# Performance work log

Measured on AMD Instinct MI355X. Metric: run time of the kernel, lower is better.

The kernel has to match this reference:

```python
import jax, jax.numpy as jnp
import numpy as np

B, MODES, L = 512, 1000, 64


def setup_inputs() -> dict:
    key = jax.random.key(0)
    ks = jax.random.split(key, 10)
    inp = {
        "params": jax.random.normal(ks[0], (B, MODES, L), dtype=jnp.float32),
        "wfft0_re": jax.random.uniform(ks[1], (L, MODES), dtype=jnp.float32),
        "wfft0_im": jax.random.uniform(ks[2], (L, MODES), dtype=jnp.float32),
        "wfft1_re": jax.random.uniform(ks[3], (L, MODES), dtype=jnp.float32),
        "wfft1_im": jax.random.uniform(ks[4], (L, MODES), dtype=jnp.float32),
        "wfft2_re": jax.random.uniform(ks[5], (L, MODES), dtype=jnp.float32),
        "wfft2_im": jax.random.uniform(ks[6], (L, MODES), dtype=jnp.float32),
        "lin1_w": jax.random.normal(ks[7], (MODES, L * MODES), dtype=jnp.float32) * 0.01,
        "lin1_b": jnp.zeros((MODES,), dtype=jnp.float32),
        "lin2_w": jax.random.normal(ks[8], (L, MODES), dtype=jnp.float32) * 0.05,
        "lin2_b": jnp.zeros((L,), dtype=jnp.float32),
    }
    return inp


def _stft_block(x, wfft):
    # x: (B, MODES, L) real or complex; wfft: (L, MODES) complex
    fx = jnp.fft.fft(x, norm="forward")            # FFT over last (layer) axis, scaled 1/L
    # Faithful to torch.einsum('bfp,mn->bfm', ...): sums over BOTH p and n
    y = jnp.einsum("bfp,mn->bfm", fx, wfft)         # (B, MODES, L)
    y = jnp.fft.ifft(y, norm="forward")             # unnormalized inverse (norm='forward')
    return jnp.tanh(y).real                         # complex tanh, then real part


def reference(params, wfft0_re, wfft0_im, wfft1_re, wfft1_im, wfft2_re, wfft2_im,
              lin1_w, lin1_b, lin2_w, lin2_b):
    w0 = wfft0_re + 1j * wfft0_im
    w1 = wfft1_re + 1j * wfft1_im
    w2 = wfft2_re + 1j * wfft2_im
    x = _stft_block(params, w0)
    x = _stft_block(x, w1)
    x = _stft_block(x, w2)
    x = x.reshape(x.shape[0], -1)                   # (B, MODES*L), row-major like torch.flatten
    x = jnp.tanh(x @ lin1_w.T + lin1_b)             # (B, MODES)
    x = jax.nn.sigmoid(x @ lin2_w.T + lin2_b)       # (B, L)
    return x
```

## Files before the change

kernel.cpp:

```cpp
#include <hip/hip_runtime.h>
#include <math.h>

#define NB 512
#define MODES 1000
#define LL 64
#define PI_D 3.14159265358979323846

#define OFF_PART   0
#define OFF_SCAL   4096
#define OFF_T2RE   4224
#define OFF_T2IM   4736
#define OFF_GP     5248
#define OFF_CNT    5504
#define OFF_W2T    16384
#define OFF_S2     2621440
#define OFF_IRR    4718592
#define OFF_E      6815744
#define OFF_SG     13107200
#define OFF_HP4    19398656
#define HP4_STRIDE 524288

__device__ __forceinline__ double retanh_d(double a, double b) {
    if (fabs(a) > 20.0) return a > 0.0 ? 1.0 : -1.0;
    double e2 = exp(2.0 * a);
    double em2 = 1.0 / e2;
    return (e2 - em2) / (e2 + em2 + 2.0 * cos(2.0 * b));
}

__global__ void k_misc(const float* __restrict__ w0r, const float* __restrict__ w0i,
                       const float* __restrict__ w1r, const float* __restrict__ w1i,
                       const float* __restrict__ w2r, const float* __restrict__ w2i,
                       const float* __restrict__ w2, char* ws) {
    int bid = blockIdx.x, t = threadIdx.x;
    if (bid < 192) {
        int k = bid >> 6, m = bid & 63;
        const float* wr = (k == 0) ? w0r : (k == 1) ? w1r : w2r;
        const float* wi = (k == 0) ? w0i : (k == 1) ? w1i : w2i;
        double sr = 0.0, si = 0.0;
        for (int c = t; c < MODES; c += 256) {
            sr += (double)wr[m * MODES + c];
            si += (double)wi[m * MODES + c];
        }
        __shared__ double lr[256], li[256];
        lr[t] = sr; li[t] = si; __syncthreads();
        for (int s = 128; s > 0; s >>= 1) {
            if (t < s) { lr[t] += lr[t + s]; li[t] += li[t + s]; }
            __syncthreads();
        }
        if (t == 0) {
            double2* p = (double2*)(ws + OFF_PART);
            p[k * 64 + m] = make_double2(lr[0], li[0]);
        }
    } else {
        int idx = (bid - 192) * 256 + t;
        int o = idx >> 6, j = idx & 63;
        ((float*)(ws + OFF_W2T))[idx] = w2[j * MODES + o];
    }
}

__global__ void k_prep(char* ws) {
    int t = threadIdx.x;
    int j = t & 63, q = t >> 6;
    double2* part = (double2*)(ws + OFF_PART);
    double* scal  = (double*)(ws + OFF_SCAL);
    double* t2re  = (double*)(ws + OFF_T2RE);
    double* t2im  = (double*)(ws + OFF_T2IM);
    float*  gp    = (float*)(ws + OFF_GP);
    __shared__ double a1[128], a2[128];
    __shared__ double sre[64], sim[64];
    __shared__ double tc[64], tsn[64];
    __shared__ double pr[4][64], pi_[4][64];
    if (t < 128) {
        double2 v = part[t];
        a1[t] = v.x; a2[t] = v.y;
    }
    if (t < 64) {
        double2 v = part[128 + t];
        sre[t] = v.x; sim[t] = v.y;
    }
    if (t >= 128 && t < 192) {
        int r = t - 128;
        double s, c;
        sincos((double)r * (PI_D / 32.0), &s, &c);
        tc[r] = c; tsn[r] = s;
    }
    __syncthreads();
    for (int s = 32; s > 0; s >>= 1) {
        if (t < 128 && (t & 63) < s) { a1[t] += a1[t + s]; a2[t] += a2[t + s]; }
        __syncthreads();
    }
    if (t < 2) { scal[2 * t] = a1[t * 64]; scal[2 * t + 1] = a2[t * 64]; }
    double tr = 0.0, ti = 0.0;
    for (int mm = q * 16; mm < q * 16 + 16; ++mm) {
        int r = (j * mm) & 63;
        double c = tc[r], s = tsn[r];
        tr += sre[mm] * c - sim[mm] * s;
        ti += sre[mm] * s + sim[mm] * c;
    }
    pr[q][j] = tr; pi_[q][j] = ti;
    __syncthreads();
    if (t < 64) {
        double trr = pr[0][t] + pr[1][t] + pr[2][t] + pr[3][t];
        double tii = pi_[0][t] + pi_[1][t] + pi_[2][t] + pi_[3][t];
        t2re[t] = trr; t2im[t] = tii;
        gp[t] = (float)retanh_d(trr, tii);
    }
    if (t == 0) *(int*)(ws + OFF_CNT) = 0;
}

__global__ void k_sE(const float* __restrict__ w1, const float* __restrict__ params,
                     char* ws) {
    int bid = blockIdx.x, t = threadIdx.x;
    if (bid < 1000) {
        int idx = bid * 512 + t;
        const double* scal = (const double*)(ws + OFF_SCAL);
        double c0r = scal[0], c0i = scal[1], c1r = scal[2], c1i = scal[3];
        float p0 = params[(size_t)idx * 64];
        double s1 = retanh_d((double)p0 * c0r, (double)p0 * c0i);
        float s1f = (float)s1;
        double s2 = retanh_d((double)s1f * c1r, (double)s1f * c1i);
        float s2f = (float)s2;
        float sg; bool irr = false;
        if (s2f == 1.0f)       sg = 1.0f;
        else if (s2f == -1.0f) sg = -1.0f;
        else { sg = (s2f >= 0.0f) ? 1.0f : -1.0f; irr = true; }
        ((float*)(ws + OFF_SG))[idx] = sg;
        ((float*)(ws + OFF_S2))[idx] = s2f;
        if (irr) {
            int pos = atomicAdd((int*)(ws + OFF_CNT), 1);
            ((int*)(ws + OFF_IRR))[pos] = idx;
        }
    } else {
        int e = bid - 1000;
        int o = e >> 3, x = e & 7;
        const float4* w4 = (const float4*)w1;
        const float4* gp4 = (const float4*)(ws + OFF_GP);
        float4 g = gp4[t & 15];
        float* E = (float*)(ws + OFF_E);
        size_t rowbase = (size_t)o * 16000;
        int cbase = x * 2048 + t;
#pragma unroll
        for (int k = 0; k < 4; ++k) {
            int gidx = cbase + k * 512;
            float a = 0.0f;
            if (gidx < 16000) {
                float4 v = w4[rowbase + gidx];
                a = v.x * g.x + v.y * g.y + v.z * g.z + v.w * g.w;
            }
            a += __shfl_xor(a, 1);
            a += __shfl_xor(a, 2);
            a += __shfl_xor(a, 4);
            a += __shfl_xor(a, 8);
            if ((t & 15) == 0) {
                int f = x * 128 + k * 32 + (t >> 4);
                E[(size_t)o * 1024 + f] = a;
            }
        }
    }
}

__global__ void k_gemm(char* ws) {
    __shared__ float As[32][68];
    __shared__ float Bs[32][68];
    const float* sgn = (const float*)(ws + OFF_SG);
    const float* E   = (const float*)(ws + OFF_E);
    float* hp4       = (float*)(ws + OFF_HP4);
    int bx = blockIdx.x;
    int by = blockIdx.y;
    int bz = blockIdx.z;
    int t = threadIdx.x;
    int tx = t & 15, ty = t >> 4;
    float acc[4][4] = {};
    const float4 z4 = make_float4(0.f, 0.f, 0.f, 0.f);
    for (int kt = 0; kt < 8; ++kt) {
        int f0 = bz * 256 + kt * 32;
#pragma unroll
        for (int p = 0; p < 2; ++p) {
            int r = (t >> 3) + p * 32;
            int c4 = t & 7;
            int f = f0 + c4 * 4;
            float4 v = (f < MODES) ? *(const float4*)(sgn + (size_t)(by * 64 + r) * MODES + f) : z4;
            As[c4 * 4 + 0][r] = v.x;
            As[c4 * 4 + 1][r] = v.y;
            As[c4 * 4 + 2][r] = v.z;
            As[c4 * 4 + 3][r] = v.w;
        }
#pragma unroll
        for (int p = 0; p < 2; ++p) {
            int r = (t >> 3) + p * 32;
            int c4 = t & 7;
            int o = bx * 64 + r;
            float4 v = (o < MODES) ? *(const float4*)(E + (size_t)o * 1024 + f0 + c4 * 4) : z4;
            Bs[c4 * 4 + 0][r] = v.x;
            Bs[c4 * 4 + 1][r] = v.y;
            Bs[c4 * 4 + 2][r] = v.z;
            Bs[c4 * 4 + 3][r] = v.w;
        }
        __syncthreads();
#pragma unroll
        for (int kk = 0; kk < 32; ++kk) {
            float4 a4 = *(const float4*)&As[kk][ty * 4];
            float4 b4 = *(const float4*)&Bs[kk][tx * 4];
            float av[4] = {a4.x, a4.y, a4.z, a4.w};
            float bv[4] = {b4.x, b4.y, b4.z, b4.w};
#pragma unroll
            for (int i = 0; i < 4; ++i)
#pragma unroll
                for (int j = 0; j < 4; ++j) acc[i][j] += av[i] * bv[j];
        }
        __syncthreads();
    }
    size_t zoff = (size_t)bz * HP4_STRIDE;
#pragma unroll
    for (int i = 0; i < 4; ++i) {
        int b = by * 64 + ty * 4 + i;
        float4 st = make_float4(acc[i][0], acc[i][1], acc[i][2], acc[i][3]);
        *(float4*)&hp4[zoff + (size_t)b * 1024 + bx * 64 + tx * 4] = st;
    }
}

__global__ void k_final(const float* __restrict__ w1, const float* __restrict__ b1,
                        const float* __restrict__ b2, float* __restrict__ out, char* ws) {
    int b = blockIdx.x, t = threadIdx.x;
    const float* hp4 = (const float*)(ws + OFF_HP4);
    __shared__ float h[MODES];
    __shared__ float part[4][64];
    __shared__ __align__(16) float cv[64];
    for (int o = t; o < MODES; o += 256) {
        size_t base = (size_t)b * 1024 + o;
        h[o] = hp4[base] + hp4[base + HP4_STRIDE] + hp4[base + 2 * HP4_STRIDE]
             + hp4[base + 3 * HP4_STRIDE] + b1[o];
    }
    __syncthreads();
    int cnt = *(const int*)(ws + OFF_CNT);
    if (cnt > 0) {
        const int* irr     = (const int*)(ws + OFF_IRR);
        const float* s2a   = (const float*)(ws + OFF_S2);
        const float* sgn   = (const float*)(ws + OFF_SG);
        const double* t2re = (const double*)(ws + OFF_T2RE);
        const double* t2im = (const double*)(ws + OFF_T2IM);
        const float* gp    = (const float*)(ws + OFF_GP);
        for (int e = 0; e < cnt; ++e) {
            int idx = irr[e];
            int bb = idx / 1000;
            if (bb != b) continue;
            int f = idx - bb * 1000;
            float s2 = s2a[idx];
            float sg = sgn[idx];
            if (t < 64) {
                double g = retanh_d((double)s2 * t2re[t], (double)s2 * t2im[t]);
                cv[t] = (float)g - sg * gp[t];
            }
            __syncthreads();
            const float4* w4 = (const float4*)w1;
            const float4* c4 = (const float4*)cv;
            for (int o = t; o < MODES; o += 256) {
                size_t base = (size_t)o * 16000 + (size_t)f * 16;
                float a = 0.0f;
#pragma unroll
                for (int r = 0; r < 16; ++r) {
                    float4 w = w4[base + r];
                    float4 c = c4[r];
                    a += w.x * c.x + w.y * c.y + w.z * c.z + w.w * c.w;
                }
                h[o] += a;
            }
            __syncthreads();
        }
    }
    for (int o = t; o < MODES; o += 256) h[o] = tanhf(h[o]);
    __syncthreads();
    const float* w2t = (const float*)(ws + OFF_W2T);
    int j = t & 63, c = t >> 6;
    float acc = 0.0f;
    for (int o = c * 250; o < c * 250 + 250; ++o) acc += h[o] * w2t[o * 64 + j];
    part[c][j] = acc;
    __syncthreads();
    if (t < 64) {
        float s = part[0][t] + part[1][t] + part[2][t] + part[3][t] + b2[t];
        out[b * 64 + t] = 1.0f / (1.0f + expf(-s));
    }
}

extern "C" void kernel_launch(void* const* d_in, const int* in_sizes, int n_in,
                              void* d_out, int out_size, void* d_ws, size_t ws_size,
                              hipStream_t stream) {
    const float* params = (const float*)d_in[0];
    const float* w0r = (const float*)d_in[1];
    const float* w0i = (const float*)d_in[2];
    const float* w1r = (const float*)d_in[3];
    const float* w1i = (const float*)d_in[4];
    const float* w2r = (const float*)d_in[5];
    const float* w2i = (const float*)d_in[6];
    const float* lin1w = (const float*)d_in[7];
    const float* lin1b = (const float*)d_in[8];
    const float* lin2w = (const float*)d_in[9];
    const float* lin2b = (const float*)d_in[10];
    char* ws = (char*)d_ws;
    float* out = (float*)d_out;

    k_misc<<<442, 256, 0, stream>>>(w0r, w0i, w1r, w1i, w2r, w2i, lin2w, ws);
    k_prep<<<1, 256, 0, stream>>>(ws);
    k_sE<<<9000, 512, 0, stream>>>(lin1w, params, ws);
    k_gemm<<<dim3(16, 8, 4), 256, 0, stream>>>(ws);
    k_final<<<512, 256, 0, stream>>>(lin1w, lin1b, lin2b, out, ws);
}
```

Baseline: 113.6 us.

## Replace FP32 SIMT GEMM with split-bf16 MFMA GEMM and drop split-K partials

E is stored as a hi/lo bf16 pair and the ±1 sign matrix as bf16. The GEMM now uses MFMA 16x16x32 bf16 instructions reading straight from global memory with no LDS staging, in place of the shared-memory FP32 4x4 register-tiled kernel. The 4-way split-K and the partial-sum buffer are removed, so k_final reads a single h buffer. Extra k_misc blocks zero the padding regions. This trades some precision (bf16 hi+lo ≈ 16-bit mantissa) for matrix-core throughput, on a GEMM that is small (512x1000x1000).

```diff
diff --git a/kernel.cpp b/kernel.cpp
--- a/kernel.cpp
+++ b/kernel.cpp
@@ -15,16 +15,26 @@
 #define OFF_W2T    16384
 #define OFF_S2     2621440
 #define OFF_IRR    4718592
-#define OFF_E      6815744
 #define OFF_SG     13107200
-#define OFF_HP4    19398656
-#define HP4_STRIDE 524288
+#define OFF_EHI    19398656
+#define OFF_ELO    21495808
+#define OFF_SGNB   23592960
+#define OFF_H      24641536
+
+typedef short short8 __attribute__((ext_vector_type(8)));
+typedef float f32x4 __attribute__((ext_vector_type(4)));
 
 __device__ __forceinline__ double retanh_d(double a, double b) {
     if (fabs(a) > 20.0) return a > 0.0 ? 1.0 : -1.0;
     double e2 = exp(2.0 * a);
     double em2 = 1.0 / e2;
     return (e2 - em2) / (e2 + em2 + 2.0 * cos(2.0 * b));
+}
+
+__device__ __forceinline__ unsigned short f2bf(float x) {
+    unsigned u = __float_as_uint(x);
+    unsigned r = (u + 0x7FFFu + ((u >> 16) & 1u)) >> 16;
+    return (unsigned short)r;
 }
 
 __global__ void k_misc(const float* __restrict__ w0r, const float* __restrict__ w0i,
@@ -51,10 +61,22 @@
             double2* p = (double2*)(ws + OFF_PART);
             p[k * 64 + m] = make_double2(lr[0], li[0]);
         }
-    } else {
+    } else if (bid < 442) {
         int idx = (bid - 192) * 256 + t;
         int o = idx >> 6, j = idx & 63;
         ((float*)(ws + OFF_W2T))[idx] = w2[j * MODES + o];
+    } else if (bid < 490) {
+        int idx = (bid - 442) * 256 + t;
+        ((unsigned*)(ws + OFF_EHI))[512000 + idx] = 0u;
+    } else if (bid < 538) {
+        int idx = (bid - 490) * 256 + t;
+        ((unsigned*)(ws + OFF_ELO))[512000 + idx] = 0u;
+    } else {
+        int idx = (bid - 538) * 256 + t;
+        if (idx < 6144) {
+            int b = idx / 12, u = idx % 12;
+            ((unsigned*)(ws + OFF_SGNB))[b * 512 + 500 + u] = 0u;
+        }
     }
 }
 
@@ -126,6 +148,9 @@
         else { sg = (s2f >= 0.0f) ? 1.0f : -1.0f; irr = true; }
         ((float*)(ws + OFF_SG))[idx] = sg;
         ((float*)(ws + OFF_S2))[idx] = s2f;
+        int b = idx / 1000, f = idx - b * 1000;
+        ((unsigned short*)(ws + OFF_SGNB))[(size_t)b * 1024 + f] =
+            (sg > 0.0f) ? (unsigned short)0x3F80 : (unsigned short)0xBF80;
         if (irr) {
             int pos = atomicAdd((int*)(ws + OFF_CNT), 1);
             ((int*)(ws + OFF_IRR))[pos] = idx;
@@ -136,7 +161,8 @@
         const float4* w4 = (const float4*)w1;
         const float4* gp4 = (const float4*)(ws + OFF_GP);
         float4 g = gp4[t & 15];
-        float* E = (float*)(ws + OFF_E);
+        unsigned short* ehi = (unsigned short*)(ws + OFF_EHI);
+        unsigned short* elo = (unsigned short*)(ws + OFF_ELO);
         size_t rowbase = (size_t)o * 16000;
         int cbase = x * 2048 + t;
 #pragma unroll
@@ -153,84 +179,60 @@
             a += __shfl_xor(a, 8);
             if ((t & 15) == 0) {
                 int f = x * 128 + k * 32 + (t >> 4);
-                E[(size_t)o * 1024 + f] = a;
+                unsigned short hi = f2bf(a);
+                float hif = __uint_as_float((unsigned)hi << 16);
+                unsigned short lo = f2bf(a - hif);
+                ehi[(size_t)o * 1024 + f] = hi;
+                elo[(size_t)o * 1024 + f] = lo;
             }
         }
     }
 }
 
-__global__ void k_gemm(char* ws) {
-    __shared__ float As[32][68];
-    __shared__ float Bs[32][68];
-    const float* sgn = (const float*)(ws + OFF_SG);
-    const float* E   = (const float*)(ws + OFF_E);
-    float* hp4       = (float*)(ws + OFF_HP4);
-    int bx = blockIdx.x;
-    int by = blockIdx.y;
-    int bz = blockIdx.z;
+__global__ void __launch_bounds__(128) k_gemm(char* ws) {
+    const unsigned short* sgnb = (const unsigned short*)(ws + OFF_SGNB);
+    const unsigned short* ehi  = (const unsigned short*)(ws + OFF_EHI);
+    const unsigned short* elo  = (const unsigned short*)(ws + OFF_ELO);
+    float* h = (float*)(ws + OFF_H);
+    int strip = blockIdx.x;
+    int btile = blockIdx.y;
     int t = threadIdx.x;
-    int tx = t & 15, ty = t >> 4;
-    float acc[4][4] = {};
-    const float4 z4 = make_float4(0.f, 0.f, 0.f, 0.f);
-    for (int kt = 0; kt < 8; ++kt) {
-        int f0 = bz * 256 + kt * 32;
+    int wave = t >> 6, l = t & 63;
+    int rc = l & 15, grp = l >> 4;
+    int b0 = btile * 16;
+    int o0 = strip * 64 + wave * 32;
+    f32x4 acc0 = {0.f, 0.f, 0.f, 0.f}, acc1 = {0.f, 0.f, 0.f, 0.f};
+    const unsigned short* ap  = sgnb + (size_t)(b0 + rc) * 1024 + grp * 8;
+    const unsigned short* bh0 = ehi + (size_t)(o0 + rc) * 1024 + grp * 8;
+    const unsigned short* bl0 = elo + (size_t)(o0 + rc) * 1024 + grp * 8;
+#pragma unroll 4
+    for (int s = 0; s < 32; ++s) {
+        short8 af  = *(const short8*)(ap + s * 32);
+        short8 h0  = *(const short8*)(bh0 + s * 32);
+        short8 l0  = *(const short8*)(bl0 + s * 32);
+        short8 h1  = *(const short8*)(bh0 + 16 * 1024 + s * 32);
+        short8 l1  = *(const short8*)(bl0 + 16 * 1024 + s * 32);
+        acc0 = __builtin_amdgcn_mfma_f32_16x16x32_bf16(af, h0, acc0, 0, 0, 0);
+        acc0 = __builtin_amdgcn_mfma_f32_16x16x32_bf16(af, l0, acc0, 0, 0, 0);
+        acc1 = __builtin_amdgcn_mfma_f32_16x16x32_bf16(af, h1, acc1, 0, 0, 0);
+        acc1 = __builtin_amdgcn_mfma_f32_16x16x32_bf16(af, l1, acc1, 0, 0, 0);
+    }
 #pragma unroll
-        for (int p = 0; p < 2; ++p) {
-            int r = (t >> 3) + p * 32;
-            int c4 = t & 7;
-            int f = f0 + c4 * 4;
-            float4 v = (f < MODES) ? *(const float4*)(sgn + (size_t)(by * 64 + r) * MODES + f) : z4;
-            As[c4 * 4 + 0][r] = v.x;
-            As[c4 * 4 + 1][r] = v.y;
-            As[c4 * 4 + 2][r] = v.z;
-            As[c4 * 4 + 3][r] = v.w;
-        }
-#pragma unroll
-        for (int p = 0; p < 2; ++p) {
-            int r = (t >> 3) + p * 32;
-            int c4 = t & 7;
-            int o = bx * 64 + r;
-            float4 v = (o < MODES) ? *(const float4*)(E + (size_t)o * 1024 + f0 + c4 * 4) : z4;
-            Bs[c4 * 4 + 0][r] = v.x;
-            Bs[c4 * 4 + 1][r] = v.y;
-            Bs[c4 * 4 + 2][r] = v.z;
-            Bs[c4 * 4 + 3][r] = v.w;
-        }
-        __syncthreads();
-#pragma unroll
-        for (int kk = 0; kk < 32; ++kk) {
-            float4 a4 = *(const float4*)&As[kk][ty * 4];
-            float4 b4 = *(const float4*)&Bs[kk][tx * 4];
-            float av[4] = {a4.x, a4.y, a4.z, a4.w};
-            float bv[4] = {b4.x, b4.y, b4.z, b4.w};
-#pragma unroll
-            for (int i = 0; i < 4; ++i)
-#pragma unroll
-                for (int j = 0; j < 4; ++j) acc[i][j] += av[i] * bv[j];
-        }
-        __syncthreads();
-    }
-    size_t zoff = (size_t)bz * HP4_STRIDE;
-#pragma unroll
-    for (int i = 0; i < 4; ++i) {
-        int b = by * 64 + ty * 4 + i;
-        float4 st = make_float4(acc[i][0], acc[i][1], acc[i][2], acc[i][3]);
-        *(float4*)&hp4[zoff + (size_t)b * 1024 + bx * 64 + tx * 4] = st;
+    for (int r = 0; r < 4; ++r) {
+        h[(size_t)(b0 + grp * 4 + r) * 1024 + o0 + rc]      = acc0[r];
+        h[(size_t)(b0 + grp * 4 + r) * 1024 + o0 + 16 + rc] = acc1[r];
     }
 }
 
 __global__ void k_final(const float* __restrict__ w1, const float* __restrict__ b1,
                         const float* __restrict__ b2, float* __restrict__ out, char* ws) {
     int b = blockIdx.x, t = threadIdx.x;
-    const float* hp4 = (const float*)(ws + OFF_HP4);
+    const float* hbuf = (const float*)(ws + OFF_H);
     __shared__ float h[MODES];
     __shared__ float part[4][64];
     __shared__ __align__(16) float cv[64];
-    for (int o = t; o < MODES; o += 256) {
-        size_t base = (size_t)b * 1024 + o;
-        h[o] = hp4[base] + hp4[base + HP4_STRIDE] + hp4[base + 2 * HP4_STRIDE]
-             + hp4[base + 3 * HP4_STRIDE] + b1[o];
-    }
+    for (int o = t; o < MODES; o += 256)
+        h[o] = hbuf[(size_t)b * 1024 + o] + b1[o];
     __syncthreads();
     int cnt = *(const int*)(ws + OFF_CNT);
     if (cnt > 0) {
@@ -299,9 +301,9 @@
     char* ws = (char*)d_ws;
     float* out = (float*)d_out;
 
-    k_misc<<<442, 256, 0, stream>>>(w0r, w0i, w1r, w1i, w2r, w2i, lin2w, ws);
+    k_misc<<<562, 256, 0, stream>>>(w0r, w0i, w1r, w1i, w2r, w2i, lin2w, ws);
     k_prep<<<1, 256, 0, stream>>>(ws);
     k_sE<<<9000, 512, 0, stream>>>(lin1w, params, ws);
-    k_gemm<<<dim3(16, 8, 4), 256, 0, stream>>>(ws);
+    k_gemm<<<dim3(16, 32), 128, 0, stream>>>(ws);
     k_final<<<512, 256, 0, stream>>>(lin1w, lin1b, lin2b, out, ws);
 }
```

After: 110.0 us (median of 2 runs). 3.1% less time.
